# Kernel optimization log

Hardware: AMD Instinct MI355X
Metric: run time of the kernel (lower is better)

## Reference

```python
import jax, jax.numpy as jnp
import numpy as np

H = 300          # node_hid_feats in GIN
DEPTH = 3        # GIN depth
B = 4096         # reactions per batch
N = 122880       # total nodes per batched graph (B * ~30 atoms)
E = 245760       # total edges per batched graph
NUM_R = 2        # reactant graphs per reaction
NUM_P = 1        # product graphs per reaction
NODE_IN = 64
EDGE_IN = 16


def setup_inputs() -> dict:
    key = jax.random.key(0)
    ks = jax.random.split(key, 20)
    inp = {}
    inp["r_x"] = jax.random.normal(ks[0], (NUM_R, N, NODE_IN), jnp.float32)
    inp["r_e"] = jax.random.normal(ks[1], (NUM_R, E, EDGE_IN), jnp.float32)
    inp["p_x"] = jax.random.normal(ks[2], (NUM_P, N, NODE_IN), jnp.float32)
    inp["p_e"] = jax.random.normal(ks[3], (NUM_P, E, EDGE_IN), jnp.float32)
    # GIN parameters (eps = 0, dropout = eval mode identity)
    inp["Wn"] = jax.random.normal(ks[4], (NODE_IN, H), jnp.float32) * (NODE_IN ** -0.5)
    inp["bn"] = jax.random.normal(ks[5], (H,), jnp.float32) * 0.02
    inp["We"] = jax.random.normal(ks[6], (EDGE_IN, H), jnp.float32) * (EDGE_IN ** -0.5)
    inp["be"] = jax.random.normal(ks[7], (H,), jnp.float32) * 0.02
    inp["W1"] = jax.random.normal(ks[8], (DEPTH, H, H), jnp.float32) * (H ** -0.5)
    inp["b1"] = jax.random.normal(ks[9], (DEPTH, H), jnp.float32) * 0.02
    inp["W2"] = jax.random.normal(ks[10], (DEPTH, H, H), jnp.float32) * (H ** -0.5)
    inp["b2"] = jax.random.normal(ks[11], (DEPTH, H), jnp.float32) * 0.02
    # graph structure (int, constant w.r.t. grads)
    inp["r_src"] = jax.random.randint(ks[12], (NUM_R, E), 0, N)
    inp["r_dst"] = jax.random.randint(ks[13], (NUM_R, E), 0, N)
    inp["r_seg"] = jnp.sort(jax.random.randint(ks[14], (NUM_R, N), 0, B), axis=-1)
    inp["p_src"] = jax.random.randint(ks[15], (NUM_P, E), 0, N)
    inp["p_dst"] = jax.random.randint(ks[16], (NUM_P, E), 0, N)
    inp["p_seg"] = jnp.sort(jax.random.randint(ks[17], (NUM_P, N), 0, B), axis=-1)
    return inp


def gin(x, e, src, dst, Wn, bn, We, be, W1, b1, W2, b2):
    """GIN forward: project -> depth x GINEConv (sum agg of relu(h_src + e))."""
    h = jax.nn.relu(x @ Wn + bn)              # [N, H]
    ef = e @ We + be                           # [E, H]
    n = x.shape[0]
    for l in range(DEPTH):
        m = jax.nn.relu(h[src] + ef)           # [E, H] edge messages
        agg = jax.ops.segment_sum(m, dst, num_segments=n)
        z = h + agg                            # (1 + eps) * h + agg, eps = 0
        h = jax.nn.relu(z @ W1[l] + b1[l]) @ W2[l] + b2[l]
        if l < DEPTH - 1:
            h = jax.nn.relu(h)
    return h


def pooled(xs, es, srcs, dsts, segs, params):
    # sum node features over all graphs in the list, pooled per reaction id
    out = jnp.zeros((B, H), jnp.float32)
    for g in range(xs.shape[0]):
        hg = gin(xs[g], es[g], srcs[g], dsts[g], *params)
        out = out + jax.ops.segment_sum(hg, segs[g], num_segments=B)
    return out


def reference(r_x, r_e, p_x, p_e, Wn, bn, We, be, W1, b1, W2, b2,
              r_src, r_dst, r_seg, p_src, p_dst, p_seg):
    params = (Wn, bn, We, be, W1, b1, W2, b2)
    r_sum = pooled(r_x, r_e, r_src, r_dst, r_seg, params)   # reactants_out
    p_sum = pooled(p_x, p_e, p_src, p_dst, p_seg, params)   # products_out
    return (r_sum - p_sum, r_sum, p_sum)
```

## Files before the change

kernel.cpp:

```cpp
#include <hip/hip_runtime.h>

typedef unsigned short u16;
typedef __attribute__((ext_vector_type(8))) short short8;
typedef __attribute__((ext_vector_type(4))) float f32x4;

#define NN 122880
#define EE 245760
#define BB 4096
#define HH 300
#define LD 320
#define NCP 384
#define WTSL (NCP * LD)
#define BHSZ (BB * HH)
#define GNB 16

__device__ __forceinline__ float b2f(u16 s) {
  union { unsigned int u; float f; } v; v.u = ((unsigned int)s) << 16; return v.f;
}
__device__ __forceinline__ u16 f2b(float f) {
  union { float f; unsigned int u; } v; v.f = f;
  unsigned int r = v.u + 0x7FFFu + ((v.u >> 16) & 1u);
  return (u16)(r >> 16);
}

__global__ __launch_bounds__(256) void prep_kernel(
    const float* __restrict__ Wn, const float* __restrict__ We,
    const float* __restrict__ W1, const float* __restrict__ W2,
    const float* __restrict__ bn, const float* __restrict__ be,
    const float* __restrict__ b1, const float* __restrict__ b2,
    u16* __restrict__ wtAll, float* __restrict__ biasAll)
{
  int idx = blockIdx.x * 256 + threadIdx.x;
  if (idx < 8 * WTSL) {
    int slot = idx / WTSL, rem = idx % WTSL;
    int n = rem / LD, k = rem % LD;
    float v = 0.f;
    if (n < HH) {
      if (slot == 0)      { if (k < 64)  v = Wn[k * HH + n]; }
      else if (slot == 1) { if (k < 16)  v = We[k * HH + n]; }
      else if (slot < 5)  { int l = slot - 2; if (k < HH) v = W1[(l * HH + k) * HH + n]; }
      else                { int l = slot - 5; if (k < HH) v = W2[(l * HH + k) * HH + n]; }
    }
    wtAll[idx] = f2b(v);
  } else {
    int j = idx - 8 * WTSL;
    if (j < 8 * NCP) {
      int slot = j / NCP, n = j % NCP;
      float v = 0.f;
      if (n < HH) {
        const float* bp = (slot == 0) ? bn : (slot == 1) ? be
                         : (slot < 5) ? (b1 + (slot - 2) * HH) : (b2 + (slot - 5) * HH);
        v = bp[n];
      }
      biasAll[j] = v;
    }
  }
}

__global__ __launch_bounds__(256) void zero_kernel(float4* __restrict__ p, int n4) {
  int i = blockIdx.x * 256 + threadIdx.x;
  if (i < n4) p[i] = make_float4(0.f, 0.f, 0.f, 0.f);
}

__global__ __launch_bounds__(256) void count_kernel(
    const int* __restrict__ dst, int* __restrict__ cursor)
{
  int e = blockIdx.x * 256 + threadIdx.x;
  if (e < EE) atomicAdd(&cursor[dst[e]], 1);
}

__global__ __launch_bounds__(1024) void scan_kernel(
    int* __restrict__ cursor, int* __restrict__ indptr)
{
  __shared__ int sd[1024];
  const int tid = threadIdx.x;
  const int base = tid * 120;
  int s = 0;
  for (int i = 0; i < 120; ++i) s += cursor[base + i];
  sd[tid] = s;
  __syncthreads();
  for (int off = 1; off < 1024; off <<= 1) {
    int v = (tid >= off) ? sd[tid - off] : 0;
    __syncthreads();
    sd[tid] += v;
    __syncthreads();
  }
  int run = sd[tid] - s;
  for (int i = 0; i < 120; ++i) {
    int c = cursor[base + i];
    indptr[base + i] = run;
    cursor[base + i] = run;
    run += c;
  }
  if (tid == 1023) indptr[NN] = run;
}

__global__ __launch_bounds__(256) void fill_kernel(
    const int* __restrict__ dst, const int* __restrict__ src,
    int* __restrict__ cursor, int2* __restrict__ ess)
{
  int e = blockIdx.x * 256 + threadIdx.x;
  if (e < EE) {
    int pos = atomicAdd(&cursor[dst[e]], 1);
    ess[pos] = make_int2(e, src[e]);
  }
}

__global__ __launch_bounds__(256) void gemm_kernel(
    const void* __restrict__ A, int lda, int K, int a_f32,
    const u16* __restrict__ WT, const float* __restrict__ bias,
    u16* __restrict__ C, int relu)
{
  __shared__ u16 As[128][40];
  __shared__ u16 Bs[160][40];

  const int tid = threadIdx.x;
  const int lane = tid & 63, w = tid >> 6;
  const int wm = (w >> 1) * 64, wn = (w & 1) * 80;
  const int m16 = lane & 15, q = lane >> 4;
  const long r0 = (long)blockIdx.x * 128;
  const int c0 = blockIdx.y * 160;

  f32x4 acc[4][5];
#pragma unroll
  for (int i = 0; i < 4; ++i)
#pragma unroll
    for (int j = 0; j < 5; ++j) acc[i][j] = (f32x4){0.f, 0.f, 0.f, 0.f};

  const int nk = K >> 5;
  for (int kt = 0; kt < nk; ++kt) {
    __syncthreads();
#pragma unroll
    for (int i = 0; i < 2; ++i) {
      int ci = tid + i * 256;
      int row = ci >> 2, kc = (ci & 3) << 3;
      int kg = (kt << 5) + kc;
      if (a_f32) {
        const float* Af = (const float*)A + (r0 + row) * (long)lda + kg;
        float4 v0 = *(const float4*)Af;
        float4 v1 = *(const float4*)(Af + 4);
        ushort4 p0, p1;
        p0.x = f2b(v0.x); p0.y = f2b(v0.y); p0.z = f2b(v0.z); p0.w = f2b(v0.w);
        p1.x = f2b(v1.x); p1.y = f2b(v1.y); p1.z = f2b(v1.z); p1.w = f2b(v1.w);
        *(ushort4*)&As[row][kc] = p0;
        *(ushort4*)&As[row][kc + 4] = p1;
      } else {
        uint4 av = *(const uint4*)((const u16*)A + (r0 + row) * (long)lda + kg);
        *(uint4*)&As[row][kc] = av;
      }
    }
#pragma unroll
    for (int i = 0; i < 3; ++i) {
      int ci = tid + i * 256;
      if (ci < 640) {
        int row = ci >> 2, kc = (ci & 3) << 3;
        int kg = (kt << 5) + kc;
        uint4 bv = *(const uint4*)(WT + (long)(c0 + row) * LD + kg);
        *(uint4*)&Bs[row][kc] = bv;
      }
    }
    __syncthreads();

    short8 af[4], bf[5];
#pragma unroll
    for (int t = 0; t < 4; ++t) af[t] = *(const short8*)&As[wm + t * 16 + m16][q << 3];
#pragma unroll
    for (int t = 0; t < 5; ++t) bf[t] = *(const short8*)&Bs[wn + t * 16 + m16][q << 3];
#pragma unroll
    for (int tm = 0; tm < 4; ++tm)
#pragma unroll
      for (int tn = 0; tn < 5; ++tn)
        acc[tm][tn] = __builtin_amdgcn_mfma_f32_16x16x32_bf16(af[tm], bf[tn], acc[tm][tn], 0, 0, 0);
  }

#pragma unroll
  for (int tn = 0; tn < 5; ++tn) {
    int c = c0 + wn + tn * 16 + m16;
    float bv = bias[c];
#pragma unroll
    for (int tm = 0; tm < 4; ++tm) {
      long rbase = r0 + wm + tm * 16 + q * 4;
#pragma unroll
      for (int i = 0; i < 4; ++i) {
        float v = acc[tm][tn][i] + bv;
        if (relu) v = v > 0.f ? v : 0.f;
        C[(rbase + i) * LD + c] = f2b(v);
      }
    }
  }
}

__global__ __launch_bounds__(320) void gather_kernel(
    const u16* __restrict__ h, const float* __restrict__ eraw,
    const u16* __restrict__ wtE, const float* __restrict__ biasE,
    const int2* __restrict__ ess, const int* __restrict__ indptr,
    u16* __restrict__ z)
{
  const int base = blockIdx.x * GNB;
  const int c = threadIdx.x;

  float wreg[16];
  {
    uint4 w0 = *(const uint4*)(wtE + (long)c * LD);
    uint4 w1 = *(const uint4*)(wtE + (long)c * LD + 8);
    const u16* pw0 = (const u16*)&w0;
    const u16* pw1 = (const u16*)&w1;
#pragma unroll
    for (int k = 0; k < 8; ++k) { wreg[k] = b2f(pw0[k]); wreg[8 + k] = b2f(pw1[k]); }
  }
  const float bv = biasE[c];

  const int t0 = indptr[base];
  const int t1 = indptr[base + GNB];

  int g = 0;
  int nxt = indptr[base + 1];
  float s = b2f(h[(long)base * LD + c]);

  for (int tb = t0; tb < t1; tb += 4) {
    const int tB = (tb + 1 < t1) ? tb + 1 : t1 - 1;
    const int tC = (tb + 2 < t1) ? tb + 2 : t1 - 1;
    const int tD = (tb + 3 < t1) ? tb + 3 : t1 - 1;
    int2 eA = ess[tb], eB = ess[tB], eC = ess[tC], eD = ess[tD];

    const float* rA = eraw + (long)eA.x * 16;
    const float* rB = eraw + (long)eB.x * 16;
    const float* rC = eraw + (long)eC.x * 16;
    const float* rD = eraw + (long)eD.x * 16;
    float4 A0 = *(const float4*)rA, A1 = *(const float4*)(rA + 4),
           A2 = *(const float4*)(rA + 8), A3 = *(const float4*)(rA + 12);
    float4 B0 = *(const float4*)rB, B1 = *(const float4*)(rB + 4),
           B2 = *(const float4*)(rB + 8), B3 = *(const float4*)(rB + 12);
    float4 C0 = *(const float4*)rC, C1 = *(const float4*)(rC + 4),
           C2 = *(const float4*)(rC + 8), C3 = *(const float4*)(rC + 12);
    float4 D0 = *(const float4*)rD, D1 = *(const float4*)(rD + 4),
           D2 = *(const float4*)(rD + 8), D3 = *(const float4*)(rD + 12);
    float hA = b2f(h[(long)eA.y * LD + c]);
    float hB = b2f(h[(long)eB.y * LD + c]);
    float hC = b2f(h[(long)eC.y * LD + c]);
    float hD = b2f(h[(long)eD.y * LD + c]);

    float mA = bv;
    mA += A0.x * wreg[0];  mA += A0.y * wreg[1];  mA += A0.z * wreg[2];  mA += A0.w * wreg[3];
    mA += A1.x * wreg[4];  mA += A1.y * wreg[5];  mA += A1.z * wreg[6];  mA += A1.w * wreg[7];
    mA += A2.x * wreg[8];  mA += A2.y * wreg[9];  mA += A2.z * wreg[10]; mA += A2.w * wreg[11];
    mA += A3.x * wreg[12]; mA += A3.y * wreg[13]; mA += A3.z * wreg[14]; mA += A3.w * wreg[15];
    mA += hA;
    float mB = bv;
    mB += B0.x * wreg[0];  mB += B0.y * wreg[1];  mB += B0.z * wreg[2];  mB += B0.w * wreg[3];
    mB += B1.x * wreg[4];  mB += B1.y * wreg[5];  mB += B1.z * wreg[6];  mB += B1.w * wreg[7];
    mB += B2.x * wreg[8];  mB += B2.y * wreg[9];  mB += B2.z * wreg[10]; mB += B2.w * wreg[11];
    mB += B3.x * wreg[12]; mB += B3.y * wreg[13]; mB += B3.z * wreg[14]; mB += B3.w * wreg[15];
    mB += hB;
    float mC = bv;
    mC += C0.x * wreg[0];  mC += C0.y * wreg[1];  mC += C0.z * wreg[2];  mC += C0.w * wreg[3];
    mC += C1.x * wreg[4];  mC += C1.y * wreg[5];  mC += C1.z * wreg[6];  mC += C1.w * wreg[7];
    mC += C2.x * wreg[8];  mC += C2.y * wreg[9];  mC += C2.z * wreg[10]; mC += C2.w * wreg[11];
    mC += C3.x * wreg[12]; mC += C3.y * wreg[13]; mC += C3.z * wreg[14]; mC += C3.w * wreg[15];
    mC += hC;
    float mD = bv;
    mD += D0.x * wreg[0];  mD += D0.y * wreg[1];  mD += D0.z * wreg[2];  mD += D0.w * wreg[3];
    mD += D1.x * wreg[4];  mD += D1.y * wreg[5];  mD += D1.z * wreg[6];  mD += D1.w * wreg[7];
    mD += D2.x * wreg[8];  mD += D2.y * wreg[9];  mD += D2.z * wreg[10]; mD += D2.w * wreg[11];
    mD += D3.x * wreg[12]; mD += D3.y * wreg[13]; mD += D3.z * wreg[14]; mD += D3.w * wreg[15];
    mD += hD;

#pragma unroll
    for (int j = 0; j < 4; ++j) {
      const float mj = (j == 0) ? mA : (j == 1) ? mB : (j == 2) ? mC : mD;
      const int t = tb + j;
      if (t < t1) {
        while (t >= nxt) {
          z[(long)(base + g) * LD + c] = f2b(s);
          ++g;
          s = b2f(h[(long)(base + g) * LD + c]);
          nxt = indptr[base + g + 1];
        }
        s += (mj > 0.f) ? mj : 0.f;
      }
    }
  }

  z[(long)(base + g) * LD + c] = f2b(s);
  for (++g; g < GNB; ++g) {
    s = b2f(h[(long)(base + g) * LD + c]);
    z[(long)(base + g) * LD + c] = f2b(s);
  }
}

__global__ __launch_bounds__(320) void pool_kernel(
    const u16* __restrict__ h, const int* __restrict__ seg, float* __restrict__ acc)
{
  int b = blockIdx.x;
  int lo, hi;
  { int l = 0, r = NN; while (l < r) { int m = (l + r) >> 1; if (seg[m] < b) l = m + 1; else r = m; } lo = l; }
  { int l = lo, r = NN; while (l < r) { int m = (l + r) >> 1; if (seg[m] < b + 1) l = m + 1; else r = m; } hi = l; }
  int j = threadIdx.x;
  if (j < HH) {
    float s = 0.f;
    for (int n = lo; n < hi; ++n) s += b2f(h[(long)n * LD + j]);
    acc[(long)b * HH + j] += s;
  }
}

__global__ __launch_bounds__(256) void combine_kernel(float* __restrict__ out) {
  int i = blockIdx.x * 256 + threadIdx.x;
  if (i < BHSZ) out[i] = out[BHSZ + i] - out[2 * BHSZ + i];
}

extern "C" void kernel_launch(void* const* d_in, const int* in_sizes, int n_in,
                              void* d_out, int out_size, void* d_ws, size_t ws_size,
                              hipStream_t stream)
{
  (void)in_sizes; (void)n_in; (void)out_size; (void)ws_size;
  const float* r_x = (const float*)d_in[0];
  const float* r_e = (const float*)d_in[1];
  const float* p_x = (const float*)d_in[2];
  const float* p_e = (const float*)d_in[3];
  const float* Wn  = (const float*)d_in[4];
  const float* bn  = (const float*)d_in[5];
  const float* We  = (const float*)d_in[6];
  const float* be  = (const float*)d_in[7];
  const float* W1  = (const float*)d_in[8];
  const float* b1  = (const float*)d_in[9];
  const float* W2  = (const float*)d_in[10];
  const float* b2  = (const float*)d_in[11];
  const int* r_src = (const int*)d_in[12];
  const int* r_dst = (const int*)d_in[13];
  const int* r_seg = (const int*)d_in[14];
  const int* p_src = (const int*)d_in[15];
  const int* p_dst = (const int*)d_in[16];
  const int* p_seg = (const int*)d_in[17];
  float* out = (float*)d_out;

  char* ws = (char*)d_ws;
  size_t off = 0;
  auto take = [&](size_t bytes) -> char* {
    char* p = ws + off;
    off = (off + bytes + 255) & ~(size_t)255;
    return p;
  };
  u16*   nb0     = (u16*)  take((size_t)NN * LD * 2);
  u16*   nb1     = (u16*)  take((size_t)NN * LD * 2);
  u16*   wtAll   = (u16*)  take((size_t)8 * WTSL * 2);
  float* biasAll = (float*)take((size_t)8 * NCP * 4);
  int*   indptr  = (int*)  take((size_t)(NN + 1) * 4);
  int*   cursor  = (int*)  take((size_t)NN * 4);
  int2*  ess     = (int2*) take((size_t)EE * 8);

  float* r_acc = out + BHSZ;
  float* p_acc = out + 2 * BHSZ;

  prep_kernel<<<3852, 256, 0, stream>>>(Wn, We, W1, W2, bn, be, b1, b2, wtAll, biasAll);
  zero_kernel<<<2400, 256, 0, stream>>>((float4*)r_acc, 614400);

  const float* xs[3] = { r_x, r_x + (size_t)NN * 64, p_x };
  const float* es[3] = { r_e, r_e + (size_t)EE * 16, p_e };
  const int* srcs[3] = { r_src, r_src + EE, p_src };
  const int* dsts[3] = { r_dst, r_dst + EE, p_dst };
  const int* segs[3] = { r_seg, r_seg + NN, p_seg };
  float*     accs[3] = { r_acc, r_acc, p_acc };

  for (int g = 0; g < 3; ++g) {
    zero_kernel<<<120, 256, 0, stream>>>((float4*)cursor, 30720);
    count_kernel<<<960, 256, 0, stream>>>(dsts[g], cursor);
    scan_kernel<<<1, 1024, 0, stream>>>(cursor, indptr);
    fill_kernel<<<960, 256, 0, stream>>>(dsts[g], srcs[g], cursor, ess);

    gemm_kernel<<<dim3(NN / 128, 2), 256, 0, stream>>>(xs[g], 64, 64, 1,
        wtAll, biasAll, nb0, 1);

    u16* hA = nb0; u16* hB = nb1;
    for (int l = 0; l < 3; ++l) {
      gather_kernel<<<NN / GNB, 320, 0, stream>>>(hA, es[g], wtAll + WTSL,
          biasAll + NCP, ess, indptr, hB);
      gemm_kernel<<<dim3(NN / 128, 2), 256, 0, stream>>>(hB, LD, LD, 0,
          wtAll + (2 + l) * WTSL, biasAll + (2 + l) * NCP, hA, 1);
      gemm_kernel<<<dim3(NN / 128, 2), 256, 0, stream>>>(hA, LD, LD, 0,
          wtAll + (5 + l) * WTSL, biasAll + (5 + l) * NCP, hB, (l < 2) ? 1 : 0);
      u16* tmp = hA; hA = hB; hB = tmp;
    }
    pool_kernel<<<BB, 320, 0, stream>>>(hA, segs[g], accs[g]);
  }
  combine_kernel<<<4800, 256, 0, stream>>>(out);
}
```

Before: 3.453 ms.

## Load GEMM fragments directly from global memory, dropping LDS staging and barriers

Each wave now loads its MFMA A and B fragments straight from global memory into registers, so the shared-memory tiles and per-k-step __syncthreads are gone. The fp32 input path is specialised to a fixed two k-steps (K=64), the bf16 path is unrolled by two, and launch bounds now request two blocks per CU. The aim is to remove LDS round trips and barrier stalls. The cost is redundant global/L2 traffic, since the waves sharing a row block or column block each reload the same data, and the fp32 path now assumes K equals 64.

```diff
diff --git a/kernel.cpp b/kernel.cpp
--- a/kernel.cpp
+++ b/kernel.cpp
@@ -106,14 +106,11 @@
   }
 }
 
-__global__ __launch_bounds__(256) void gemm_kernel(
+__global__ __launch_bounds__(256, 2) void gemm_kernel(
     const void* __restrict__ A, int lda, int K, int a_f32,
     const u16* __restrict__ WT, const float* __restrict__ bias,
     u16* __restrict__ C, int relu)
 {
-  __shared__ u16 As[128][40];
-  __shared__ u16 Bs[160][40];
-
   const int tid = threadIdx.x;
   const int lane = tid & 63, w = tid >> 6;
   const int wm = (w >> 1) * 64, wn = (w & 1) * 80;
@@ -128,49 +125,50 @@
     for (int j = 0; j < 5; ++j) acc[i][j] = (f32x4){0.f, 0.f, 0.f, 0.f};
 
   const int nk = K >> 5;
-  for (int kt = 0; kt < nk; ++kt) {
-    __syncthreads();
-#pragma unroll
-    for (int i = 0; i < 2; ++i) {
-      int ci = tid + i * 256;
-      int row = ci >> 2, kc = (ci & 3) << 3;
-      int kg = (kt << 5) + kc;
-      if (a_f32) {
-        const float* Af = (const float*)A + (r0 + row) * (long)lda + kg;
-        float4 v0 = *(const float4*)Af;
-        float4 v1 = *(const float4*)(Af + 4);
-        ushort4 p0, p1;
-        p0.x = f2b(v0.x); p0.y = f2b(v0.y); p0.z = f2b(v0.z); p0.w = f2b(v0.w);
-        p1.x = f2b(v1.x); p1.y = f2b(v1.y); p1.z = f2b(v1.z); p1.w = f2b(v1.w);
-        *(ushort4*)&As[row][kc] = p0;
-        *(ushort4*)&As[row][kc + 4] = p1;
-      } else {
-        uint4 av = *(const uint4*)((const u16*)A + (r0 + row) * (long)lda + kg);
-        *(uint4*)&As[row][kc] = av;
+  const u16* Bb = WT + (long)(c0 + wn + m16) * LD + (q << 3);
+
+  if (a_f32) {
+    const float* Ab = (const float*)A + (r0 + wm + m16) * (long)lda + (q << 3);
+#pragma unroll
+    for (int kt = 0; kt < 2; ++kt) {
+      const int kg = kt << 5;
+      short8 af[4], bf[5];
+#pragma unroll
+      for (int t = 0; t < 4; ++t) {
+        const float* ap = Ab + (long)t * 16 * lda + kg;
+        float4 v0 = *(const float4*)ap;
+        float4 v1 = *(const float4*)(ap + 4);
+        short8 r;
+        r[0] = (short)f2b(v0.x); r[1] = (short)f2b(v0.y);
+        r[2] = (short)f2b(v0.z); r[3] = (short)f2b(v0.w);
+        r[4] = (short)f2b(v1.x); r[5] = (short)f2b(v1.y);
+        r[6] = (short)f2b(v1.z); r[7] = (short)f2b(v1.w);
+        af[t] = r;
       }
-    }
-#pragma unroll
-    for (int i = 0; i < 3; ++i) {
-      int ci = tid + i * 256;
-      if (ci < 640) {
-        int row = ci >> 2, kc = (ci & 3) << 3;
-        int kg = (kt << 5) + kc;
-        uint4 bv = *(const uint4*)(WT + (long)(c0 + row) * LD + kg);
-        *(uint4*)&Bs[row][kc] = bv;
-      }
-    }
-    __syncthreads();
-
-    short8 af[4], bf[5];
-#pragma unroll
-    for (int t = 0; t < 4; ++t) af[t] = *(const short8*)&As[wm + t * 16 + m16][q << 3];
-#pragma unroll
-    for (int t = 0; t < 5; ++t) bf[t] = *(const short8*)&Bs[wn + t * 16 + m16][q << 3];
-#pragma unroll
-    for (int tm = 0; tm < 4; ++tm)
-#pragma unroll
-      for (int tn = 0; tn < 5; ++tn)
-        acc[tm][tn] = __builtin_amdgcn_mfma_f32_16x16x32_bf16(af[tm], bf[tn], acc[tm][tn], 0, 0, 0);
+#pragma unroll
+      for (int t = 0; t < 5; ++t) bf[t] = *(const short8*)(Bb + (long)t * 16 * LD + kg);
+#pragma unroll
+      for (int tm = 0; tm < 4; ++tm)
+#pragma unroll
+        for (int tn = 0; tn < 5; ++tn)
+          acc[tm][tn] = __builtin_amdgcn_mfma_f32_16x16x32_bf16(af[tm], bf[tn], acc[tm][tn], 0, 0, 0);
+    }
+  } else {
+    const u16* Ab = (const u16*)A + (r0 + wm + m16) * (long)lda + (q << 3);
+#pragma unroll 2
+    for (int kt = 0; kt < nk; ++kt) {
+      const int kg = kt << 5;
+      short8 af[4], bf[5];
+#pragma unroll
+      for (int t = 0; t < 4; ++t) af[t] = *(const short8*)(Ab + (long)t * 16 * lda + kg);
+#pragma unroll
+      for (int t = 0; t < 5; ++t) bf[t] = *(const short8*)(Bb + (long)t * 16 * LD + kg);
+#pragma unroll
+      for (int tm = 0; tm < 4; ++tm)
+#pragma unroll
+        for (int tn = 0; tn < 5; ++tn)
+          acc[tm][tn] = __builtin_amdgcn_mfma_f32_16x16x32_bf16(af[tm], bf[tn], acc[tm][tn], 0, 0, 0);
+    }
   }
 
 #pragma unroll
```

New measurement: 3.747 ms. +8.5%, slower.
